# Optimization experiments

Measured on AMD Instinct MI355X. Metric: run time of the kernel, lower is better.

## Reference

```python
import jax, jax.numpy as jnp
import numpy as np

N_NODES = 100000
N_EDGES = 1000000
F_IN = 32       # CFG.feature_dim
H = 64          # CFG.hidden_dim
H2 = 2 * H      # L1 family: conv1 out = hidden_dim * 2
N_GRAPHS = 64


def gcn_conv(x, src, dst, deg_inv_sqrt, W, b, num_nodes):
    # PyG GCNConv: out = D^{-1/2} (A + I) D^{-1/2} (x @ W) + b
    h = x @ W  # [N, out]
    norm = (deg_inv_sqrt[src] * deg_inv_sqrt[dst])[:, None]  # [E+N, 1]
    msg = h[src] * norm
    return jax.ops.segment_sum(msg, dst, num_segments=num_nodes) + b


def setup_inputs() -> dict:
    key = jax.random.key(0)
    ks = jax.random.split(key, 10)
    x = jax.random.normal(ks[0], (N_NODES, F_IN), dtype=jnp.float32)
    edge_index = jax.random.randint(ks[1], (2, N_EDGES), 0, N_NODES, dtype=jnp.int64)
    batch = jnp.sort(jax.random.randint(ks[2], (N_NODES,), 0, N_GRAPHS, dtype=jnp.int64))
    def glorot(k, shape):
        lim = np.sqrt(6.0 / (shape[0] + shape[1]))
        return jax.random.uniform(k, shape, jnp.float32, -lim, lim)
    W1 = glorot(ks[3], (F_IN, H2))
    b1 = jnp.zeros((H2,), jnp.float32)
    W2 = glorot(ks[4], (H2, H))
    b2 = jnp.zeros((H,), jnp.float32)
    Wrt = glorot(ks[5], (H, H))
    brt = jnp.zeros((H,), jnp.float32)
    return {"x": x, "edge_index": edge_index, "batch": batch,
            "W1": W1, "b1": b1, "W2": W2, "b2": b2, "Wrt": Wrt, "brt": brt}


def reference(x, edge_index, batch, W1, b1, W2, b2, Wrt, brt):
    num_nodes = x.shape[0]
    loop = jnp.arange(num_nodes, dtype=edge_index.dtype)
    src = jnp.concatenate([edge_index[0], loop])  # add self-loops
    dst = jnp.concatenate([edge_index[1], loop])
    deg = jax.ops.segment_sum(jnp.ones_like(dst, dtype=x.dtype), dst, num_segments=num_nodes)
    deg_inv_sqrt = jnp.where(deg > 0, jax.lax.rsqrt(deg), 0.0)

    h = jax.nn.relu(gcn_conv(x, src, dst, deg_inv_sqrt, W1, b1, num_nodes))
    h = gcn_conv(h, src, dst, deg_inv_sqrt, W2, b2, num_nodes)
    h = h @ Wrt + brt  # L1 reverse transcriptase

    # global_mean_pool over batch segments
    sums = jax.ops.segment_sum(h, batch, num_segments=N_GRAPHS)
    counts = jax.ops.segment_sum(jnp.ones((num_nodes,), h.dtype), batch, num_segments=N_GRAPHS)
    pooled = sums / jnp.maximum(counts, 1.0)[:, None]

    activity_factor = 1.0  # age = 0 -> 1/(1+0)
    return pooled * activity_factor
```

## Files before the change

kernel.cpp:

```cpp
#include <hip/hip_runtime.h>

#define NN 100000
#define NE 1000000
#define FIN 32
#define H2 128
#define HH 64
#define NG 64
#define SLOT 16
#define OSLOT 48

#define BSH 9
#define BNODES 512
#define NB 196
#define CAPL 28
#define CAPB 6144
#define CHUNK 2048
#define NSPILL 4096
#define ZN (NN + NG + NG * HH + 256 + 64)

typedef __attribute__((ext_vector_type(8))) short short8;
typedef __attribute__((ext_vector_type(4))) float f32x4;
typedef __attribute__((ext_vector_type(2))) float f32x2;

__device__ __forceinline__ unsigned f2bf(float f) {
    unsigned u = __float_as_uint(f);
    return (u + 0x7FFFu + ((u >> 16) & 1u)) >> 16;
}
__device__ __forceinline__ float bf2f(unsigned u) {
    return __uint_as_float(u << 16);
}
__device__ __forceinline__ void dec8(float* a, float w, uint2 v) {
    f32x2 p0 = __builtin_amdgcn_cvt_pk_f32_fp8((int)v.x, false);
    f32x2 p1 = __builtin_amdgcn_cvt_pk_f32_fp8((int)v.x, true);
    f32x2 p2 = __builtin_amdgcn_cvt_pk_f32_fp8((int)v.y, false);
    f32x2 p3 = __builtin_amdgcn_cvt_pk_f32_fp8((int)v.y, true);
    a[0] = fmaf(w, p0.x, a[0]); a[1] = fmaf(w, p0.y, a[1]);
    a[2] = fmaf(w, p1.x, a[2]); a[3] = fmaf(w, p1.y, a[3]);
    a[4] = fmaf(w, p2.x, a[4]); a[5] = fmaf(w, p2.y, a[5]);
    a[6] = fmaf(w, p3.x, a[6]); a[7] = fmaf(w, p3.y, a[7]);
}
__device__ __forceinline__ unsigned char f2fp8(float f) {
    return (unsigned char)(__builtin_amdgcn_cvt_pk_fp8_f32(f, f, 0, false) & 0xff);
}

__global__ void k_setup(const float* __restrict__ x, const float* __restrict__ W1,
                        const float* __restrict__ W2, const float* __restrict__ Wrt,
                        const float* __restrict__ b2, const float* __restrict__ brt,
                        int* __restrict__ zws, uint2* __restrict__ xb8,
                        unsigned short* __restrict__ w2t, float* __restrict__ brt2,
                        unsigned short* __restrict__ w1t) {
    int i = blockIdx.x * 256 + threadIdx.x;
    if (i < ZN) zws[i] = 0;
    if (i < NN * FIN / 8) {
        float4 a = ((const float4*)x)[2 * i];
        float4 b = ((const float4*)x)[2 * i + 1];
        unsigned u0 = __builtin_amdgcn_cvt_pk_fp8_f32(a.x, a.y, 0, false);
        u0 = __builtin_amdgcn_cvt_pk_fp8_f32(a.z, a.w, u0, true);
        unsigned u1 = __builtin_amdgcn_cvt_pk_fp8_f32(b.x, b.y, 0, false);
        u1 = __builtin_amdgcn_cvt_pk_fp8_f32(b.z, b.w, u1, true);
        xb8[i] = make_uint2(u0, u1);
    }
    if (i < H2 * HH) {
        int r = i >> 6, c = i & 63;
        float acc = 0.f;
        for (int k = 0; k < HH; ++k) acc = fmaf(W2[r * HH + k], Wrt[k * HH + c], acc);
        w2t[c * H2 + r] = (unsigned short)f2bf(acc);
    } else if (i < H2 * HH + HH) {
        int c = i - H2 * HH;
        float acc = brt[c];
        for (int k = 0; k < HH; ++k) acc = fmaf(b2[k], Wrt[k * HH + c], acc);
        brt2[c] = acc;
    } else if (i < H2 * HH + HH + FIN * H2) {
        int j = i - (H2 * HH + HH);
        int k = j >> 7, c = j & 127;
        w1t[c * FIN + k] = (unsigned short)f2bf(W1[j]);
    }
}

__global__ __launch_bounds__(256) void k_bin(const int* __restrict__ ei,
                                             int* __restrict__ gcnt,
                                             unsigned* __restrict__ gbuf,
                                             int* __restrict__ gspillc,
                                             int* __restrict__ gspill) {
    __shared__ int cur[NB];
    __shared__ int gbase[NB];
    __shared__ unsigned stage[NB * CAPL];
    for (int i = threadIdx.x; i < NB; i += 256) cur[i] = 0;
    __syncthreads();
    int e0 = blockIdx.x * CHUNK;
#pragma unroll
    for (int it = 0; it < CHUNK / 256; ++it) {
        int e = e0 + it * 256 + threadIdx.x;
        if (e < NE) {
            int d = ei[NE + e];
            int b = d >> BSH;
            unsigned u = ((unsigned)ei[e] << BSH) | (unsigned)(d & (BNODES - 1));
            int p = atomicAdd(&cur[b], 1);
            if (p < CAPL) stage[b * CAPL + p] = u;
            else {
                int q = atomicAdd(gspillc, 1);
                if (q < NSPILL) { gspill[2 * q] = b; gspill[2 * q + 1] = (int)u; }
            }
        }
    }
    __syncthreads();
    if (threadIdx.x < NB) {
        int len = min(cur[threadIdx.x], CAPL);
        gbase[threadIdx.x] = len ? atomicAdd(&gcnt[threadIdx.x], len) : 0;
    }
    __syncthreads();
    int wid = threadIdx.x >> 6, lane = threadIdx.x & 63;
    for (int b = wid; b < NB; b += 4) {
        int len = min(cur[b], CAPL);
        if (len == 0) continue;
        int base = gbase[b];
        if (base + len > CAPB) len = max(0, CAPB - base);
        if (lane < len)
            gbuf[(size_t)b * CAPB + base + lane] = stage[b * CAPL + lane];
    }
}

__global__ __launch_bounds__(512) void k_build(const unsigned* __restrict__ gbuf,
                                               const int* __restrict__ gcnt,
                                               const int* __restrict__ gspillc,
                                               const int* __restrict__ gspill,
                                               const int* __restrict__ bat,
                                               int* __restrict__ esrc,
                                               int* __restrict__ ovf,
                                               int* __restrict__ fill,
                                               float* __restrict__ dis,
                                               int* __restrict__ counts) {
    __shared__ int cnt[BNODES];
    __shared__ int slots[BNODES * SLOT];
    for (int i = threadIdx.x; i < BNODES; i += 512) cnt[i] = 0;
    __syncthreads();
    int b = blockIdx.x;
    int len = min(gcnt[b], CAPB);
    const unsigned* buf = gbuf + (size_t)b * CAPB;
    for (int i = threadIdx.x; i < len; i += 512) {
        unsigned u = buf[i];
        int ln = u & (BNODES - 1);
        int src = (int)(u >> BSH);
        int p = atomicAdd(&cnt[ln], 1);
        if (p < SLOT) slots[ln * SLOT + p] = src;
        else if (p < SLOT + OSLOT)
            ovf[(size_t)(b * BNODES + ln) * OSLOT + (p - SLOT)] = src;
    }
    int ns = min(*gspillc, NSPILL);
    for (int i = threadIdx.x; i < ns; i += 512) {
        if (gspill[2 * i] == b) {
            unsigned u = (unsigned)gspill[2 * i + 1];
            int ln = u & (BNODES - 1);
            int src = (int)(u >> BSH);
            int p = atomicAdd(&cnt[ln], 1);
            if (p < SLOT) slots[ln * SLOT + p] = src;
            else if (p < SLOT + OSLOT)
                ovf[(size_t)(b * BNODES + ln) * OSLOT + (p - SLOT)] = src;
        }
    }
    __syncthreads();
    int nbase = b * BNODES;
    int nvalid = min(BNODES, NN - nbase);
    if (nvalid <= 0) return;
    {
        int li = threadIdx.x;
        bool v = li < nvalid;
        int n = nbase + li;
        if (v) {
            int c = cnt[li];
            fill[n] = c;
            dis[n] = rsqrtf((float)(c + 1));
        }
        int lane = li & 63;
        int g = v ? bat[n] : -1;
        int gprev = __shfl_up(g, 1, 64);
        bool head = (lane == 0) || (g != gprev);
        unsigned long long hm = __ballot(head && v);
        int gnext = __shfl_down(g, 1, 64);
        bool tail = v && ((lane == 63) || (gnext != g));
        if (tail) {
            unsigned long long below =
                (lane == 63) ? ~0ull : ((1ull << (lane + 1)) - 1ull);
            int start = 63 - __clzll(hm & below);
            atomicAdd(&counts[g], lane - start + 1);
        }
    }
    int nwords = nvalid * SLOT / 4;
    int4* d4 = (int4*)(esrc + (size_t)nbase * SLOT);
    const int4* s4 = (const int4*)slots;
    for (int i = threadIdx.x; i < nwords; i += 512) d4[i] = s4[i];
}

__global__ void k_pack(const int* __restrict__ cnt, const float* __restrict__ dis,
                       int* __restrict__ esrc, int* __restrict__ ovf) {
    int i = blockIdx.x * 256 + threadIdx.x;
    if (i < NN * SLOT) {
        int n = i >> 4, p = i & 15;
        if (p < min(cnt[n], SLOT)) {
            int s = esrc[i];
            esrc[i] = (int)(((unsigned)s << 15) | (f2bf(dis[s]) & 0x7FFFu));
        }
    } else if (i < NN * SLOT + NN) {
        int n = i - NN * SLOT;
        int c = cnt[n];
        if (c > SLOT) {
            int cov = min(c - SLOT, OSLOT);
            int* orow = ovf + (size_t)n * OSLOT;
            for (int q = 0; q < cov; ++q) {
                int s = orow[q];
                orow[q] = (int)(((unsigned)s << 15) | (f2bf(dis[s]) & 0x7FFFu));
            }
        }
    }
}

__global__ __launch_bounds__(256) void k_mlpg(
    const uint2* __restrict__ xb8, const float* __restrict__ dis,
    const int* __restrict__ cnt, const int* __restrict__ esrc,
    const int* __restrict__ ovf,
    const unsigned short* __restrict__ w1tg, const unsigned short* __restrict__ w2tg,
    const float* __restrict__ b1, unsigned char* __restrict__ y) {
    __shared__ unsigned short w1t[H2 * FIN];
    __shared__ unsigned short w2t[HH * H2];
    __shared__ float b1s[H2];
    __shared__ float h1s[4][16 * 132];
    __shared__ __align__(16) unsigned short aggs[4][16 * 40];
    for (int i = threadIdx.x; i < FIN * H2 / 8; i += 256)
        ((uint4*)w1t)[i] = ((const uint4*)w1tg)[i];
    for (int i = threadIdx.x; i < HH * H2 / 8; i += 256)
        ((uint4*)w2t)[i] = ((const uint4*)w2tg)[i];
    if (threadIdx.x < H2) b1s[threadIdx.x] = b1[threadIdx.x];
    __syncthreads();
    int wid = threadIdx.x >> 6, l = threadIdx.x & 63;
    int base = (blockIdx.x * 4 + wid) * 16;
    if (base >= NN) return;

    {
        int n = base + (l >> 2), t = l & 3;
        float dn = dis[n];
        float a[8] = {0.f, 0.f, 0.f, 0.f, 0.f, 0.f, 0.f, 0.f};
        dec8(a, dn * dn, xb8[(size_t)n * 4 + t]);
        int c = cnt[n];
        int c1 = min(c, SLOT);
        if (c1 > 0) {
            const int4* rp = (const int4*)(esrc + (size_t)n * SLOT);
            int4 i0 = rp[0], i1 = rp[1], i2 = rp[2], i3 = rp[3];
            int ej[16] = {i0.x, i0.y, i0.z, i0.w, i1.x, i1.y, i1.z, i1.w,
                          i2.x, i2.y, i2.z, i2.w, i3.x, i3.y, i3.z, i3.w};
            int e0 = i0.x;
#pragma unroll
            for (int j = 0; j < 16; ++j) {
                int e = (j < c1) ? ej[j] : e0;
                int s = (int)((unsigned)e >> 15);
                float w = (j < c1) ? bf2f(e & 0x7FFF) * dn : 0.f;
                dec8(a, w, xb8[(size_t)s * 4 + t]);
            }
        }
        if (c > SLOT) {
            int cov = min(c - SLOT, OSLOT);
            const int* orow = ovf + (size_t)n * OSLOT;
            for (int p = 0; p < cov; ++p) {
                int e = orow[p];
                int s = (int)((unsigned)e >> 15);
                dec8(a, bf2f(e & 0x7FFF) * dn, xb8[(size_t)s * 4 + t]);
            }
        }
        uint4 r;
        r.x = f2bf(a[0]) | (f2bf(a[1]) << 16);
        r.y = f2bf(a[2]) | (f2bf(a[3]) << 16);
        r.z = f2bf(a[4]) | (f2bf(a[5]) << 16);
        r.w = f2bf(a[6]) | (f2bf(a[7]) << 16);
        *(uint4*)(&aggs[wid][(l >> 2) * 40 + t * 8]) = r;
    }

    int lr = l & 15, lk = l >> 4;
    float* h1w = h1s[wid];
    const f32x4 zero = {0.f, 0.f, 0.f, 0.f};

    short8 a1 = *(const short8*)(&aggs[wid][lr * 40 + lk * 8]);
#pragma unroll
    for (int ct = 0; ct < 8; ++ct) {
        short8 bf = *(const short8*)&w1t[(ct * 16 + lr) * FIN + lk * 8];
        f32x4 c = __builtin_amdgcn_mfma_f32_16x16x32_bf16(a1, bf, zero, 0, 0, 0);
        float bv = b1s[ct * 16 + lr];
#pragma unroll
        for (int q = 0; q < 4; ++q)
            h1w[(lk * 4 + q) * 132 + ct * 16 + lr] = fmaxf(c[q] + bv, 0.f);
    }

    f32x4 acc0 = zero, acc1 = zero, acc2 = zero, acc3 = zero;
#pragma unroll
    for (int kt = 0; kt < 4; ++kt) {
        const float* ap = &h1w[lr * 132 + kt * 32 + lk * 8];
        float4 alo = *(const float4*)ap;
        float4 ahi = *(const float4*)(ap + 4);
        short8 af;
        af[0] = (short)f2bf(alo.x); af[1] = (short)f2bf(alo.y);
        af[2] = (short)f2bf(alo.z); af[3] = (short)f2bf(alo.w);
        af[4] = (short)f2bf(ahi.x); af[5] = (short)f2bf(ahi.y);
        af[6] = (short)f2bf(ahi.z); af[7] = (short)f2bf(ahi.w);
        const unsigned short* wb = &w2t[lr * H2 + kt * 32 + lk * 8];
        short8 b0 = *(const short8*)(wb);
        short8 b1f = *(const short8*)(wb + 16 * H2);
        short8 b2f = *(const short8*)(wb + 32 * H2);
        short8 b3f = *(const short8*)(wb + 48 * H2);
        acc0 = __builtin_amdgcn_mfma_f32_16x16x32_bf16(af, b0, acc0, 0, 0, 0);
        acc1 = __builtin_amdgcn_mfma_f32_16x16x32_bf16(af, b1f, acc1, 0, 0, 0);
        acc2 = __builtin_amdgcn_mfma_f32_16x16x32_bf16(af, b2f, acc2, 0, 0, 0);
        acc3 = __builtin_amdgcn_mfma_f32_16x16x32_bf16(af, b3f, acc3, 0, 0, 0);
    }
    unsigned char* ybs = (unsigned char*)h1w;
#pragma unroll
    for (int q = 0; q < 4; ++q) {
        int r = lk * 4 + q;
        ybs[r * 64 + lr +  0] = f2fp8(acc0[q]);
        ybs[r * 64 + lr + 16] = f2fp8(acc1[q]);
        ybs[r * 64 + lr + 32] = f2fp8(acc2[q]);
        ybs[r * 64 + lr + 48] = f2fp8(acc3[q]);
    }
    ((uint4*)(y + (size_t)base * 64))[l] = ((const uint4*)ybs)[l];
}

__global__ __launch_bounds__(256, 4) void k_l2g(
    const uint2* __restrict__ y2, const float* __restrict__ dis,
    const int* __restrict__ cnt, const int* __restrict__ esrc,
    const int* __restrict__ ovf, const float* __restrict__ brt2,
    const int* __restrict__ bat, float* __restrict__ pool) {
    __shared__ float hred[32][HH];
    __shared__ int gids[32];
    int idx = blockIdx.x * 256 + threadIdx.x;
    int n = idx >> 3;
    int t = threadIdx.x & 7;
    int ni = threadIdx.x >> 3;
    float dn = dis[n];
    float a[8];
    {
        float4 blo = ((const float4*)brt2)[t * 2];
        float4 bhi = ((const float4*)brt2)[t * 2 + 1];
        a[0] = blo.x; a[1] = blo.y; a[2] = blo.z; a[3] = blo.w;
        a[4] = bhi.x; a[5] = bhi.y; a[6] = bhi.z; a[7] = bhi.w;
        dec8(a, dn * dn, y2[(size_t)n * 8 + t]);
    }
    int c = cnt[n];
    int c1 = min(c, SLOT);
    if (c1 > 0) {
        const int4* rp = (const int4*)(esrc + (size_t)n * SLOT);
        int4 i0 = rp[0], i1 = rp[1], i2 = rp[2], i3 = rp[3];
        int ej[16] = {i0.x, i0.y, i0.z, i0.w, i1.x, i1.y, i1.z, i1.w,
                      i2.x, i2.y, i2.z, i2.w, i3.x, i3.y, i3.z, i3.w};
        int e0 = i0.x;
#pragma unroll
        for (int j = 0; j < 16; ++j) {
            int e = (j < c1) ? ej[j] : e0;
            int s = (int)((unsigned)e >> 15);
            float w = (j < c1) ? bf2f(e & 0x7FFF) * dn : 0.f;
            dec8(a, w, y2[(size_t)s * 8 + t]);
        }
    }
    if (c > SLOT) {
        int cov = min(c - SLOT, OSLOT);
        const int* orow = ovf + (size_t)n * OSLOT;
        for (int p = 0; p < cov; ++p) {
            int e = orow[p];
            int s = (int)((unsigned)e >> 15);
            dec8(a, bf2f(e & 0x7FFF) * dn, y2[(size_t)s * 8 + t]);
        }
    }
    ((float4*)&hred[ni][t * 8])[0] = make_float4(a[0], a[1], a[2], a[3]);
    ((float4*)&hred[ni][t * 8])[1] = make_float4(a[4], a[5], a[6], a[7]);
    if (t == 0) gids[ni] = bat[n];
    __syncthreads();
    if (threadIdx.x < HH) {
        int f = threadIdx.x;
        int cg = gids[0];
        float s = 0.f;
        for (int j = 0; j < 32; ++j) {
            int g = gids[j];
            if (g != cg) { atomicAdd(&pool[cg * HH + f], s); s = 0.f; cg = g; }
            s += hred[j][f];
        }
        atomicAdd(&pool[cg * HH + f], s);
    }
}

__global__ void k_final(const float* __restrict__ pool, const int* __restrict__ counts,
                        float* __restrict__ out) {
    int i = blockIdx.x * 256 + threadIdx.x;
    if (i < NG * HH) {
        int g = i >> 6;
        out[i] = pool[i] / fmaxf((float)counts[g], 1.0f);
    }
}


extern "C" void kernel_launch(void* const* d_in, const int* in_sizes, int n_in,
                              void* d_out, int out_size, void* d_ws, size_t ws_size,
                              hipStream_t stream) {
    const float* x   = (const float*)d_in[0];
    const int*   ei  = (const int*)d_in[1];
    const int*   bat = (const int*)d_in[2];
    const float* W1  = (const float*)d_in[3];
    const float* b1  = (const float*)d_in[4];
    const float* W2  = (const float*)d_in[5];
    const float* b2  = (const float*)d_in[6];
    const float* Wrt = (const float*)d_in[7];
    const float* brt = (const float*)d_in[8];
    float* out = (float*)d_out;

    int* ws = (int*)d_ws;
    int* fill    = ws;
    int* counts  = ws + NN;
    float* pool  = (float*)(ws + NN + NG);
    int* gcnt    = ws + NN + NG + NG * HH;
    int* gspillc = gcnt + 256;
    int* gspill  = ws + ZN;
    float* dis   = (float*)(gspill + 2 * NSPILL);
    int* esrc    = (int*)dis + NN;
    int* ovf     = esrc + (size_t)NN * SLOT;
    unsigned* gbuf = (unsigned*)(ovf + (size_t)NN * OSLOT);
    uint2* xb8     = (uint2*)(gbuf + (size_t)NB * CAPB);
    unsigned char* yb = (unsigned char*)((unsigned*)xb8 + NN * 8);
    unsigned short* w1t = (unsigned short*)(yb + (size_t)NN * 64);
    unsigned short* w2t = w1t + FIN * H2;
    float* brt2 = (float*)(w2t + H2 * HH);

    k_setup<<<(NN * FIN / 8 + 255) / 256, 256, 0, stream>>>(
        x, W1, W2, Wrt, b2, brt, ws, xb8, w2t, brt2, w1t);
    k_bin<<<(NE + CHUNK - 1) / CHUNK, 256, 0, stream>>>(ei, gcnt, gbuf, gspillc, gspill);
    k_build<<<NB, 512, 0, stream>>>(gbuf, gcnt, gspillc, gspill, bat,
                                    esrc, ovf, fill, dis, counts);
    k_pack<<<(NN * (SLOT + 1) + 255) / 256, 256, 0, stream>>>(fill, dis, esrc, ovf);
    k_mlpg<<<(NN + 63) / 64, 256, 0, stream>>>(
        xb8, dis, fill, esrc, ovf, w1t, w2t, b1, yb);
    k_l2g<<<NN * 8 / 256, 256, 0, stream>>>(
        (const uint2*)yb, dis, fill, esrc, ovf, brt2, bat, pool);
    k_final<<<(NG * HH + 255) / 256, 256, 0, stream>>>(pool, counts, out);
}
```

Baseline: 98.04 us.

## Split layer-2 features into two column halves to shrink the gather working set

k_mlpg now writes its fp8 output as two separate 32-column arrays, each with a 32-byte row. k_l2g runs one grid per half, so each gather pass touches a table half the size, which should fit better in L2. In exchange, the edge index and overflow lists are read twice, once per slice. The pool atomics use column offsets. The per-node fill array is also moved out of the region zeroed in k_setup, which drops NN stores on the assumption that k_build writes every entry.

```diff
diff --git a/kernel.cpp b/kernel.cpp
--- a/kernel.cpp
+++ b/kernel.cpp
@@ -16,7 +16,8 @@
 #define CAPB 6144
 #define CHUNK 2048
 #define NSPILL 4096
-#define ZN (NN + NG + NG * HH + 256 + 64)
+#define ZN2 (NG + NG * HH + 256 + 64)
+#define NBLK2 3125
 
 typedef __attribute__((ext_vector_type(8))) short short8;
 typedef __attribute__((ext_vector_type(4))) float f32x4;
@@ -39,6 +40,12 @@
     a[4] = fmaf(w, p2.x, a[4]); a[5] = fmaf(w, p2.y, a[5]);
     a[6] = fmaf(w, p3.x, a[6]); a[7] = fmaf(w, p3.y, a[7]);
 }
+__device__ __forceinline__ void dec4(float* a, float w, unsigned v) {
+    f32x2 p0 = __builtin_amdgcn_cvt_pk_f32_fp8((int)v, false);
+    f32x2 p1 = __builtin_amdgcn_cvt_pk_f32_fp8((int)v, true);
+    a[0] = fmaf(w, p0.x, a[0]); a[1] = fmaf(w, p0.y, a[1]);
+    a[2] = fmaf(w, p1.x, a[2]); a[3] = fmaf(w, p1.y, a[3]);
+}
 __device__ __forceinline__ unsigned char f2fp8(float f) {
     return (unsigned char)(__builtin_amdgcn_cvt_pk_fp8_f32(f, f, 0, false) & 0xff);
 }
@@ -50,7 +57,7 @@
                         unsigned short* __restrict__ w2t, float* __restrict__ brt2,
                         unsigned short* __restrict__ w1t) {
     int i = blockIdx.x * 256 + threadIdx.x;
-    if (i < ZN) zws[i] = 0;
+    if (i < ZN2) zws[i] = 0;
     if (i < NN * FIN / 8) {
         float4 a = ((const float4*)x)[2 * i];
         float4 b = ((const float4*)x)[2 * i + 1];
@@ -219,7 +226,8 @@
     const int* __restrict__ cnt, const int* __restrict__ esrc,
     const int* __restrict__ ovf,
     const unsigned short* __restrict__ w1tg, const unsigned short* __restrict__ w2tg,
-    const float* __restrict__ b1, unsigned char* __restrict__ y) {
+    const float* __restrict__ b1,
+    unsigned char* __restrict__ y_lo, unsigned char* __restrict__ y_hi) {
     __shared__ unsigned short w1t[H2 * FIN];
     __shared__ unsigned short w2t[HH * H2];
     __shared__ float b1s[H2];
@@ -318,28 +326,38 @@
         ybs[r * 64 + lr + 32] = f2fp8(acc2[q]);
         ybs[r * 64 + lr + 48] = f2fp8(acc3[q]);
     }
-    ((uint4*)(y + (size_t)base * 64))[l] = ((const uint4*)ybs)[l];
+    {
+        int k = l & 31;
+        int row = k >> 1;
+        int off = (k & 1) * 16;
+        const uint4* src = (const uint4*)(ybs + row * 64 + ((l >= 32) ? 32 : 0) + off);
+        unsigned char* dst = ((l < 32) ? y_lo : y_hi) + (size_t)(base + row) * 32 + off;
+        *(uint4*)dst = *src;
+    }
 }
 
 __global__ __launch_bounds__(256, 4) void k_l2g(
-    const uint2* __restrict__ y2, const float* __restrict__ dis,
-    const int* __restrict__ cnt, const int* __restrict__ esrc,
-    const int* __restrict__ ovf, const float* __restrict__ brt2,
-    const int* __restrict__ bat, float* __restrict__ pool) {
-    __shared__ float hred[32][HH];
+    const unsigned* __restrict__ ylo, const unsigned* __restrict__ yhi,
+    const float* __restrict__ dis, const int* __restrict__ cnt,
+    const int* __restrict__ esrc, const int* __restrict__ ovf,
+    const float* __restrict__ brt2, const int* __restrict__ bat,
+    float* __restrict__ pool) {
+    __shared__ float hred[32][32];
     __shared__ int gids[32];
-    int idx = blockIdx.x * 256 + threadIdx.x;
-    int n = idx >> 3;
-    int t = threadIdx.x & 7;
-    int ni = threadIdx.x >> 3;
+    int slice = blockIdx.x / NBLK2;
+    int nb = blockIdx.x - slice * NBLK2;
+    const unsigned* yh = slice ? yhi : ylo;
+    int scol = slice * 32;
+    int tid = threadIdx.x;
+    int n = nb * 32 + (tid >> 3);
+    int t = tid & 7;
+    int ni = tid >> 3;
     float dn = dis[n];
-    float a[8];
+    float a[4];
     {
-        float4 blo = ((const float4*)brt2)[t * 2];
-        float4 bhi = ((const float4*)brt2)[t * 2 + 1];
-        a[0] = blo.x; a[1] = blo.y; a[2] = blo.z; a[3] = blo.w;
-        a[4] = bhi.x; a[5] = bhi.y; a[6] = bhi.z; a[7] = bhi.w;
-        dec8(a, dn * dn, y2[(size_t)n * 8 + t]);
+        float4 bv = *(const float4*)(brt2 + scol + t * 4);
+        a[0] = bv.x; a[1] = bv.y; a[2] = bv.z; a[3] = bv.w;
+        dec4(a, dn * dn, yh[(size_t)n * 8 + t]);
     }
     int c = cnt[n];
     int c1 = min(c, SLOT);
@@ -354,7 +372,7 @@
             int e = (j < c1) ? ej[j] : e0;
             int s = (int)((unsigned)e >> 15);
             float w = (j < c1) ? bf2f(e & 0x7FFF) * dn : 0.f;
-            dec8(a, w, y2[(size_t)s * 8 + t]);
+            dec4(a, w, yh[(size_t)s * 8 + t]);
         }
     }
     if (c > SLOT) {
@@ -363,23 +381,22 @@
         for (int p = 0; p < cov; ++p) {
             int e = orow[p];
             int s = (int)((unsigned)e >> 15);
-            dec8(a, bf2f(e & 0x7FFF) * dn, y2[(size_t)s * 8 + t]);
-        }
-    }
-    ((float4*)&hred[ni][t * 8])[0] = make_float4(a[0], a[1], a[2], a[3]);
-    ((float4*)&hred[ni][t * 8])[1] = make_float4(a[4], a[5], a[6], a[7]);
+            dec4(a, bf2f(e & 0x7FFF) * dn, yh[(size_t)s * 8 + t]);
+        }
+    }
+    *(float4*)&hred[ni][t * 4] = make_float4(a[0], a[1], a[2], a[3]);
     if (t == 0) gids[ni] = bat[n];
     __syncthreads();
-    if (threadIdx.x < HH) {
-        int f = threadIdx.x;
+    if (tid < 32) {
+        int f = tid;
         int cg = gids[0];
         float s = 0.f;
         for (int j = 0; j < 32; ++j) {
             int g = gids[j];
-            if (g != cg) { atomicAdd(&pool[cg * HH + f], s); s = 0.f; cg = g; }
+            if (g != cg) { atomicAdd(&pool[cg * HH + scol + f], s); s = 0.f; cg = g; }
             s += hred[j][f];
         }
-        atomicAdd(&pool[cg * HH + f], s);
+        atomicAdd(&pool[cg * HH + scol + f], s);
     }
 }
 
@@ -408,19 +425,20 @@
     float* out = (float*)d_out;
 
     int* ws = (int*)d_ws;
-    int* fill    = ws;
-    int* counts  = ws + NN;
-    float* pool  = (float*)(ws + NN + NG);
-    int* gcnt    = ws + NN + NG + NG * HH;
+    int* counts  = ws;
+    float* pool  = (float*)(ws + NG);
+    int* gcnt    = ws + NG + NG * HH;
     int* gspillc = gcnt + 256;
-    int* gspill  = ws + ZN;
+    int* fill    = ws + ZN2;
+    int* gspill  = fill + NN;
     float* dis   = (float*)(gspill + 2 * NSPILL);
     int* esrc    = (int*)dis + NN;
     int* ovf     = esrc + (size_t)NN * SLOT;
     unsigned* gbuf = (unsigned*)(ovf + (size_t)NN * OSLOT);
     uint2* xb8     = (uint2*)(gbuf + (size_t)NB * CAPB);
-    unsigned char* yb = (unsigned char*)((unsigned*)xb8 + NN * 8);
-    unsigned short* w1t = (unsigned short*)(yb + (size_t)NN * 64);
+    unsigned char* y_lo = (unsigned char*)((unsigned*)xb8 + NN * 8);
+    unsigned char* y_hi = y_lo + (size_t)NN * 32;
+    unsigned short* w1t = (unsigned short*)(y_hi + (size_t)NN * 32);
     unsigned short* w2t = w1t + FIN * H2;
     float* brt2 = (float*)(w2t + H2 * HH);
 
@@ -431,8 +449,9 @@
                                     esrc, ovf, fill, dis, counts);
     k_pack<<<(NN * (SLOT + 1) + 255) / 256, 256, 0, stream>>>(fill, dis, esrc, ovf);
     k_mlpg<<<(NN + 63) / 64, 256, 0, stream>>>(
-        xb8, dis, fill, esrc, ovf, w1t, w2t, b1, yb);
-    k_l2g<<<NN * 8 / 256, 256, 0, stream>>>(
-        (const uint2*)yb, dis, fill, esrc, ovf, brt2, bat, pool);
+        xb8, dis, fill, esrc, ovf, w1t, w2t, b1, y_lo, y_hi);
+    k_l2g<<<NBLK2 * 2, 256, 0, stream>>>(
+        (const unsigned*)y_lo, (const unsigned*)y_hi, dis, fill, esrc, ovf,
+        brt2, bat, pool);
     k_final<<<(NG * HH + 255) / 256, 256, 0, stream>>>(pool, counts, out);
 }
```

After: 105.1 us. +7.2%, slower.
